# Kernel tuning notes

Measured on AMD Instinct MI355X. Metric: run time of the kernel, lower is better.

The kernel has to match this reference:

```python
import jax, jax.numpy as jnp
import numpy as np

T, H, F, E, K = 4096, 1024, 4096, 8, 2


def setup_inputs() -> dict:
    key = jax.random.key(0)
    ks = jax.random.split(key, 6)
    hidden_states = jax.random.normal(ks[0], (T, H), dtype=jnp.float32)
    expert_weights = jax.random.uniform(ks[1], (T, K), dtype=jnp.float32)
    selected_experts = jax.random.randint(ks[2], (T, K), 0, E, dtype=jnp.int64)
    W1 = 0.02 * jax.random.normal(ks[3], (E, H, F), dtype=jnp.float32)
    b1 = jnp.zeros((E, F), dtype=jnp.float32)
    W2 = 0.02 * jax.random.normal(ks[4], (E, F, H), dtype=jnp.float32)
    b2 = jnp.zeros((E, H), dtype=jnp.float32)
    return {"hidden_states": hidden_states, "expert_weights": expert_weights,
            "W1": W1, "b1": b1, "W2": W2, "b2": b2,
            "selected_experts": selected_experts}


def reference(hidden_states, expert_weights, W1, b1, W2, b2, selected_experts):
    # Combine weight per (token, expert): sum of routing weights over top-k
    # slots assigned to that expert; slots with expert_idx < 0 contribute 0.
    num_experts = W1.shape[0]
    onehot = (selected_experts[:, :, None] == jnp.arange(num_experts)[None, None, :])
    valid = (selected_experts >= 0)[:, :, None]
    cw = jnp.einsum('tk,tke->te', expert_weights,
                    (onehot & valid).astype(hidden_states.dtype))  # [T, E]

    out = jnp.zeros_like(hidden_states)
    for e in range(num_experts):  # small fixed expert count
        h = jax.nn.gelu(hidden_states @ W1[e] + b1[e], approximate=False)  # [T, F]
        y = h @ W2[e] + b2[e]                                              # [T, H]
        out = out + cw[:, e:e + 1] * y
    return out
```

## Files before the change

kernel.cpp:

```cpp
#include <hip/hip_runtime.h>
#include <hip/hip_bf16.h>

#define Td 4096
#define Hd 1024
#define Fd 4096
#define Ed 8
#define Rcap 10240

typedef __attribute__((ext_vector_type(8))) short bf16x8;
typedef __attribute__((ext_vector_type(4))) float f32x4;
typedef __attribute__((ext_vector_type(8))) unsigned short u16x8;

__device__ __forceinline__ unsigned short f32_to_bf16(float x) {
  unsigned int u = __float_as_uint(x);
  unsigned int r = (u + 0x7FFFu + ((u >> 16) & 1u)) >> 16;
  return (unsigned short)r;
}

__device__ __forceinline__ void gload_lds16(const unsigned short* g, unsigned short* l) {
  __builtin_amdgcn_global_load_lds(
      (const __attribute__((address_space(1))) unsigned int*)g,
      (__attribute__((address_space(3))) unsigned int*)l, 16, 0, 0);
}

__global__ __launch_bounds__(256) void cvt_bf16_kernel(const float* __restrict__ in,
                                                       unsigned short* __restrict__ outp, int n8) {
  int i = blockIdx.x * 256 + threadIdx.x;
  if (i >= n8) return;
  const float4* p = (const float4*)(in + (size_t)i * 8);
  float4 a = p[0], b = p[1];
  u16x8 o;
  o[0] = f32_to_bf16(a.x); o[1] = f32_to_bf16(a.y); o[2] = f32_to_bf16(a.z); o[3] = f32_to_bf16(a.w);
  o[4] = f32_to_bf16(b.x); o[5] = f32_to_bf16(b.y); o[6] = f32_to_bf16(b.z); o[7] = f32_to_bf16(b.w);
  *(u16x8*)(outp + (size_t)i * 8) = o;
}

__global__ __launch_bounds__(256) void transpose_cvt_kernel(const float* __restrict__ in,
                                                            unsigned short* __restrict__ outp,
                                                            int Rdm, int Cdm) {
  __shared__ float tile[64][68];
  int tilesR = Rdm >> 6, tilesC = Cdm >> 6;
  int per = tilesR * tilesC;
  int bid = blockIdx.x;
  int e = bid / per; int rem = bid - e * per;
  int tr = rem / tilesC; int tc = rem - tr * tilesC;
  int r0 = tr << 6, c0 = tc << 6;
  int tid = threadIdx.x;
  int rr = tid >> 2, cq = (tid & 3) << 4;
  const float* src = in + ((size_t)e * Rdm + r0 + rr) * Cdm + c0 + cq;
  float4 v0 = ((const float4*)src)[0];
  float4 v1 = ((const float4*)src)[1];
  float4 v2 = ((const float4*)src)[2];
  float4 v3 = ((const float4*)src)[3];
  *(float4*)&tile[rr][cq + 0]  = v0;
  *(float4*)&tile[rr][cq + 4]  = v1;
  *(float4*)&tile[rr][cq + 8]  = v2;
  *(float4*)&tile[rr][cq + 12] = v3;
  __syncthreads();
  u16x8 o0, o1;
#pragma unroll
  for (int j = 0; j < 8; j++) o0[j] = f32_to_bf16(tile[cq + j][rr]);
#pragma unroll
  for (int j = 0; j < 8; j++) o1[j] = f32_to_bf16(tile[cq + 8 + j][rr]);
  unsigned short* dst = outp + ((size_t)e * Cdm + c0 + rr) * Rdm + r0 + cq;
  *(u16x8*)dst = o0;
  *(u16x8*)(dst + 8) = o1;
}

__global__ __launch_bounds__(1024) void route_all_kernel(const int* __restrict__ sel,
                                                         const float* __restrict__ ew,
                                                         int* __restrict__ idxT,
                                                         float* __restrict__ wgtT,
                                                         int* __restrict__ off_g,
                                                         int* __restrict__ cidx,
                                                         float* __restrict__ cwgt) {
  __shared__ int cnt[Ed];
  __shared__ int off[Ed + 1];
  int tid = threadIdx.x;
  if (tid < Ed) cnt[tid] = 0;
  __syncthreads();
  for (int t = tid; t < Td; t += 1024) {
    int e0 = sel[2 * t], e1 = sel[2 * t + 1];
    float w0 = ew[2 * t], w1 = ew[2 * t + 1];
    if (e0 == e1) { w0 += w1; e1 = -1; }
    if (e0 >= 0 && e0 < Ed) { int p = atomicAdd(&cnt[e0], 1); idxT[e0 * Td + p] = t; wgtT[e0 * Td + p] = w0; }
    if (e1 >= 0 && e1 < Ed) { int p = atomicAdd(&cnt[e1], 1); idxT[e1 * Td + p] = t; wgtT[e1 * Td + p] = w1; }
  }
  __syncthreads();
  if (tid == 0) {
    int acc = 0; off[0] = 0;
#pragma unroll
    for (int e = 0; e < Ed; e++) { acc += (cnt[e] + 255) & ~255; off[e + 1] = acc; }
  }
  __syncthreads();
  for (int j = tid; j < Ed * Td; j += 1024) {
    int e = j >> 12, i = j & (Td - 1);
    int row = off[e] + i;
    if (row < off[e + 1]) {
      if (i < cnt[e]) { cidx[row] = idxT[e * Td + i]; cwgt[row] = wgtT[e * Td + i]; }
      else            { cidx[row] = -1;               cwgt[row] = 0.f; }
    }
  }
  if (tid <= Ed) off_g[tid] = off[tid];
}

template <bool FIRST, int KD, int NC, int KSPLIT>
__global__ __launch_bounds__(512, 2) void gemm_kernel(const unsigned short* __restrict__ Abase,
                                                      const unsigned short* __restrict__ Bt,
                                                      const float* __restrict__ bias,
                                                      const int* __restrict__ cidx,
                                                      const float* __restrict__ cwgt,
                                                      const int* __restrict__ off,
                                                      unsigned short* __restrict__ hbuf,
                                                      float* __restrict__ outp) {
  extern __shared__ unsigned short lds[];
  constexpr int KLEN = KD / KSPLIT;
  constexpr int NT = KLEN / 64;

  const int row0 = blockIdx.x << 8;
  const int tot = off[Ed];
  if (row0 >= tot) return;
  int e = 0;
  while (off[e + 1] <= row0) ++e;
  const int n0 = blockIdx.y << 7;
  const int kbase = blockIdx.z * KLEN;

  const int tid = threadIdx.x;
  const int lane = tid & 63, w = tid >> 6;
  const int wrow = w >> 2, wcol = w & 3;
  const int fr = lane & 15;
  const int fkb = (lane >> 4) << 4;

  const unsigned short* aptr[4];
#pragma unroll
  for (int i = 0; i < 4; i++) {
    int r = (i << 6) + (tid >> 3);
    int kel = ((tid & 7) ^ (r & 7)) << 3;
    int g;
    if (FIRST) { g = cidx[row0 + r]; if (g < 0) g = 0; }
    else       { g = row0 + r; }
    aptr[i] = Abase + (size_t)g * KD + kbase + kel;
  }
  const unsigned short* bptr[2];
#pragma unroll
  for (int i = 0; i < 2; i++) {
    int r = (i << 6) + (tid >> 3);
    int kel = ((tid & 7) ^ (r & 7)) << 3;
    bptr[i] = Bt + ((size_t)e * NC + n0 + r) * KD + kbase + kel;
  }
  unsigned short* ldsA = lds;
  unsigned short* ldsB = lds + 49152;

  f32x4 acc[8][2] = {};

#define STAGE(t)                                                         \
  {                                                                      \
    int _b = (t) % 3;                                                    \
    int _k0 = (t) << 6;                                                  \
    unsigned short* _la = ldsA + (_b << 14) + (w << 9);                  \
    unsigned short* _lb = ldsB + (_b << 13) + (w << 9);                  \
    _Pragma("unroll")                                                    \
    for (int _i = 0; _i < 4; _i++) gload_lds16(aptr[_i] + _k0, _la + (_i << 12)); \
    _Pragma("unroll")                                                    \
    for (int _i = 0; _i < 2; _i++) gload_lds16(bptr[_i] + _k0, _lb + (_i << 12)); \
  }

#define LDA(dst, buf, m, ks)                                                     \
  {                                                                              \
    int _r = (wrow << 7) + ((m) << 4) + fr;                                      \
    int _p = (((ks) << 6) + fkb) ^ ((_r & 7) << 4);                              \
    dst = *(const bf16x8*)(ldsA + ((buf) << 14) + (_r << 6) + (_p >> 1));        \
  }
#define LDB(dst, buf, nf, ks)                                                    \
  {                                                                              \
    int _r = (wcol << 5) + ((nf) << 4) + fr;                                     \
    int _p = (((ks) << 6) + fkb) ^ ((_r & 7) << 4);                              \
    dst = *(const bf16x8*)(ldsB + ((buf) << 13) + (_r << 6) + (_p >> 1));        \
  }

  STAGE(0);
  if constexpr (NT > 1) {
    STAGE(1);
    asm volatile("s_waitcnt vmcnt(6)" ::: "memory");
  } else {
    asm volatile("s_waitcnt vmcnt(0)" ::: "memory");
  }
  __builtin_amdgcn_s_barrier();

  for (int t = 0; t < NT; ++t) {
    const int buf = t % 3;
    bf16x8 bfr[2][2];
#pragma unroll
    for (int nf = 0; nf < 2; nf++)
#pragma unroll
      for (int ks = 0; ks < 2; ks++) LDB(bfr[nf][ks], buf, nf, ks);
    bf16x8 afr[4][2];
#pragma unroll
    for (int m = 0; m < 4; m++)
#pragma unroll
      for (int ks = 0; ks < 2; ks++) LDA(afr[m][ks], buf, m, ks);
    if (t + 2 < NT) STAGE(t + 2);
    __builtin_amdgcn_s_barrier();
    __builtin_amdgcn_s_setprio(1);
#pragma unroll
    for (int m = 0; m < 4; m++)
#pragma unroll
      for (int nf = 0; nf < 2; nf++)
#pragma unroll
        for (int ks = 0; ks < 2; ks++)
          acc[m][nf] = __builtin_amdgcn_mfma_f32_16x16x32_bf16(afr[m][ks], bfr[nf][ks], acc[m][nf], 0, 0, 0);
    __builtin_amdgcn_s_setprio(0);
    __builtin_amdgcn_s_barrier();
#pragma unroll
    for (int m = 0; m < 4; m++)
#pragma unroll
      for (int ks = 0; ks < 2; ks++) LDA(afr[m][ks], buf, m + 4, ks);
    __builtin_amdgcn_s_barrier();
    __builtin_amdgcn_s_setprio(1);
#pragma unroll
    for (int m = 0; m < 4; m++)
#pragma unroll
      for (int nf = 0; nf < 2; nf++)
#pragma unroll
        for (int ks = 0; ks < 2; ks++)
          acc[m + 4][nf] = __builtin_amdgcn_mfma_f32_16x16x32_bf16(afr[m][ks], bfr[nf][ks], acc[m + 4][nf], 0, 0, 0);
    __builtin_amdgcn_s_setprio(0);
    if (t + 2 < NT) { asm volatile("s_waitcnt vmcnt(6)" ::: "memory"); }
    else            { asm volatile("s_waitcnt vmcnt(0)" ::: "memory"); }
    __builtin_amdgcn_s_barrier();
  }
#undef STAGE
#undef LDA
#undef LDB

  if (FIRST) {
    float bv[2];
#pragma unroll
    for (int nf = 0; nf < 2; nf++) bv[nf] = bias[e * NC + n0 + (wcol << 5) + (nf << 4) + fr];
#pragma unroll
    for (int m = 0; m < 8; m++) {
#pragma unroll
      for (int r2 = 0; r2 < 4; r2++) {
        int row = row0 + (wrow << 7) + (m << 4) + ((lane >> 4) << 2) + r2;
#pragma unroll
        for (int nf = 0; nf < 2; nf++) {
          int col = n0 + (wcol << 5) + (nf << 4) + fr;
          float x = acc[m][nf][r2] + bv[nf];
          float g = 0.5f * x * (1.0f + erff(x * 0.70710678118654752f));
          hbuf[(size_t)row * NC + col] = f32_to_bf16(g);
        }
      }
    }
  } else {
    float bv[2];
#pragma unroll
    for (int nf = 0; nf < 2; nf++)
      bv[nf] = (blockIdx.z == 0) ? bias[e * NC + n0 + (wcol << 5) + (nf << 4) + fr] : 0.f;
#pragma unroll
    for (int m = 0; m < 8; m++) {
#pragma unroll
      for (int r2 = 0; r2 < 4; r2++) {
        int row = row0 + (wrow << 7) + (m << 4) + ((lane >> 4) << 2) + r2;
        int tdst = cidx[row];
        float cw = cwgt[row];
        if (tdst >= 0) {
#pragma unroll
          for (int nf = 0; nf < 2; nf++) {
            int col = n0 + (wcol << 5) + (nf << 4) + fr;
            atomicAdd(outp + (size_t)tdst * NC + col, cw * (acc[m][nf][r2] + bv[nf]));
          }
        }
      }
    }
  }
}

extern "C" void kernel_launch(void* const* d_in, const int* in_sizes, int n_in,
                              void* d_out, int out_size, void* d_ws, size_t ws_size,
                              hipStream_t stream) {
  const float* hidden = (const float*)d_in[0];
  const float* ew     = (const float*)d_in[1];
  const float* W1     = (const float*)d_in[2];
  const float* b1     = (const float*)d_in[3];
  const float* W2     = (const float*)d_in[4];
  const float* b2     = (const float*)d_in[5];
  const int*   sel    = (const int*)d_in[6];
  float* outp = (float*)d_out;

  unsigned short* hbf  = (unsigned short*)d_ws;
  unsigned short* W1T  = hbf + (size_t)Td * Hd;
  unsigned short* W2T  = W1T + (size_t)Ed * Fd * Hd;
  unsigned short* hbuf = W2T + (size_t)Ed * Hd * Fd;
  int*   idxT = (int*)(hbuf + (size_t)Rcap * Fd);
  float* wgtT = (float*)(idxT + Ed * Td);
  int*   off  = (int*)(wgtT + Ed * Td);
  int*   cidx = off + 16;
  float* cwgt = (float*)(cidx + Rcap);

  constexpr int LDS_BYTES = 147456;
  (void)hipFuncSetAttribute((const void*)gemm_kernel<true, Hd, Fd, 1>,
                            hipFuncAttributeMaxDynamicSharedMemorySize, LDS_BYTES);
  (void)hipFuncSetAttribute((const void*)gemm_kernel<false, Fd, Hd, 2>,
                            hipFuncAttributeMaxDynamicSharedMemorySize, LDS_BYTES);

  (void)hipMemsetAsync(d_out, 0, (size_t)Td * Hd * sizeof(float), stream);

  cvt_bf16_kernel<<<(Td * Hd / 8 + 255) / 256, 256, 0, stream>>>(hidden, hbf, Td * Hd / 8);
  transpose_cvt_kernel<<<Ed * (Hd / 64) * (Fd / 64), 256, 0, stream>>>(W1, W1T, Hd, Fd);
  transpose_cvt_kernel<<<Ed * (Fd / 64) * (Hd / 64), 256, 0, stream>>>(W2, W2T, Fd, Hd);

  route_all_kernel<<<1, 1024, 0, stream>>>(sel, ew, idxT, wgtT, off, cidx, cwgt);

  gemm_kernel<true, Hd, Fd, 1><<<dim3(Rcap / 256, Fd / 128, 1), 512, LDS_BYTES, stream>>>(
      hbf, W1T, b1, cidx, cwgt, off, hbuf, nullptr);
  gemm_kernel<false, Fd, Hd, 2><<<dim3(Rcap / 256, Hd / 128, 2), 512, LDS_BYTES, stream>>>(
      hbuf, W2T, b2, cidx, cwgt, off, nullptr, outp);
}
```

Measured before the change: 658.8 us.

## Replace atomic scatter with per-row output plus combine kernel, retile GEMM warps

```diff
diff --git a/kernel.cpp b/kernel.cpp
--- a/kernel.cpp
+++ b/kernel.cpp
@@ -70,64 +70,77 @@
 __global__ __launch_bounds__(1024) void route_all_kernel(const int* __restrict__ sel,
                                                          const float* __restrict__ ew,
                                                          int* __restrict__ idxT,
-                                                         float* __restrict__ wgtT,
                                                          int* __restrict__ off_g,
                                                          int* __restrict__ cidx,
-                                                         float* __restrict__ cwgt) {
+                                                         int2* __restrict__ trow,
+                                                         float2* __restrict__ twgt) {
   __shared__ int cnt[Ed];
   __shared__ int off[Ed + 1];
   int tid = threadIdx.x;
   if (tid < Ed) cnt[tid] = 0;
   __syncthreads();
-  for (int t = tid; t < Td; t += 1024) {
+  int2 pks[Td / 1024];
+#pragma unroll
+  for (int k = 0; k < Td / 1024; k++) {
+    int t = tid + (k << 10);
     int e0 = sel[2 * t], e1 = sel[2 * t + 1];
     float w0 = ew[2 * t], w1 = ew[2 * t + 1];
     if (e0 == e1) { w0 += w1; e1 = -1; }
-    if (e0 >= 0 && e0 < Ed) { int p = atomicAdd(&cnt[e0], 1); idxT[e0 * Td + p] = t; wgtT[e0 * Td + p] = w0; }
-    if (e1 >= 0 && e1 < Ed) { int p = atomicAdd(&cnt[e1], 1); idxT[e1 * Td + p] = t; wgtT[e1 * Td + p] = w1; }
+    int2 pk = make_int2(-1, -1);
+    if (e0 >= 0 && e0 < Ed) { int p = atomicAdd(&cnt[e0], 1); idxT[e0 * Td + p] = t; pk.x = (p << 3) | e0; }
+    if (e1 >= 0 && e1 < Ed) { int p = atomicAdd(&cnt[e1], 1); idxT[e1 * Td + p] = t; pk.y = (p << 3) | e1; }
+    pks[k] = pk;
+    twgt[t] = make_float2(w0, w1);
   }
   __syncthreads();
   if (tid == 0) {
-    int acc = 0; off[0] = 0;
-#pragma unroll
-    for (int e = 0; e < Ed; e++) { acc += (cnt[e] + 255) & ~255; off[e + 1] = acc; }
+    int a = 0; off[0] = 0;
+#pragma unroll
+    for (int e = 0; e < Ed; e++) { a += (cnt[e] + 255) & ~255; off[e + 1] = a; }
   }
   __syncthreads();
+#pragma unroll
+  for (int k = 0; k < Td / 1024; k++) {
+    int t = tid + (k << 10);
+    int2 pk = pks[k];
+    int2 r;
+    r.x = (pk.x >= 0) ? off[pk.x & 7] + (pk.x >> 3) : -1;
+    r.y = (pk.y >= 0) ? off[pk.y & 7] + (pk.y >> 3) : -1;
+    trow[t] = r;
+  }
   for (int j = tid; j < Ed * Td; j += 1024) {
     int e = j >> 12, i = j & (Td - 1);
     int row = off[e] + i;
-    if (row < off[e + 1]) {
-      if (i < cnt[e]) { cidx[row] = idxT[e * Td + i]; cwgt[row] = wgtT[e * Td + i]; }
-      else            { cidx[row] = -1;               cwgt[row] = 0.f; }
-    }
+    if (row < off[e + 1]) cidx[row] = (i < cnt[e]) ? idxT[e * Td + i] : -1;
   }
   if (tid <= Ed) off_g[tid] = off[tid];
 }
 
-template <bool FIRST, int KD, int NC, int KSPLIT>
-__global__ __launch_bounds__(512, 2) void gemm_kernel(const unsigned short* __restrict__ Abase,
+template <bool FIRST, int KD, int NC, int MAP>
+__global__ __launch_bounds__(512, 1) void gemm_kernel(const unsigned short* __restrict__ Abase,
                                                       const unsigned short* __restrict__ Bt,
                                                       const float* __restrict__ bias,
                                                       const int* __restrict__ cidx,
-                                                      const float* __restrict__ cwgt,
                                                       const int* __restrict__ off,
                                                       unsigned short* __restrict__ hbuf,
-                                                      float* __restrict__ outp) {
+                                                      float* __restrict__ yout) {
   extern __shared__ unsigned short lds[];
-  constexpr int KLEN = KD / KSPLIT;
-  constexpr int NT = KLEN / 64;
-
-  const int row0 = blockIdx.x << 8;
+  constexpr int NT = KD / 64;
+
+  const int xcd = blockIdx.x & 7, slot = blockIdx.x >> 3;
+  int mt, nt;
+  if (MAP == 0) { nt = (xcd << 2) + (slot & 3); mt = slot >> 2; }
+  else          { nt = slot & 7;                mt = xcd * 5 + (slot >> 3); }
+  const int row0 = mt << 8;
   const int tot = off[Ed];
   if (row0 >= tot) return;
   int e = 0;
   while (off[e + 1] <= row0) ++e;
-  const int n0 = blockIdx.y << 7;
-  const int kbase = blockIdx.z * KLEN;
+  const int n0 = nt << 7;
 
   const int tid = threadIdx.x;
   const int lane = tid & 63, w = tid >> 6;
-  const int wrow = w >> 2, wcol = w & 3;
+  const int wrow = w >> 1, wcol = w & 1;
   const int fr = lane & 15;
   const int fkb = (lane >> 4) << 4;
 
@@ -139,140 +152,132 @@
     int g;
     if (FIRST) { g = cidx[row0 + r]; if (g < 0) g = 0; }
     else       { g = row0 + r; }
-    aptr[i] = Abase + (size_t)g * KD + kbase + kel;
+    aptr[i] = Abase + (size_t)g * KD + kel;
   }
   const unsigned short* bptr[2];
 #pragma unroll
   for (int i = 0; i < 2; i++) {
     int r = (i << 6) + (tid >> 3);
     int kel = ((tid & 7) ^ (r & 7)) << 3;
-    bptr[i] = Bt + ((size_t)e * NC + n0 + r) * KD + kbase + kel;
+    bptr[i] = Bt + ((size_t)e * NC + n0 + r) * KD + kel;
   }
   unsigned short* ldsA = lds;
   unsigned short* ldsB = lds + 49152;
 
-  f32x4 acc[8][2] = {};
-
-#define STAGE(t)                                                         \
-  {                                                                      \
-    int _b = (t) % 3;                                                    \
-    int _k0 = (t) << 6;                                                  \
-    unsigned short* _la = ldsA + (_b << 14) + (w << 9);                  \
-    unsigned short* _lb = ldsB + (_b << 13) + (w << 9);                  \
-    _Pragma("unroll")                                                    \
-    for (int _i = 0; _i < 4; _i++) gload_lds16(aptr[_i] + _k0, _la + (_i << 12)); \
-    _Pragma("unroll")                                                    \
-    for (int _i = 0; _i < 2; _i++) gload_lds16(bptr[_i] + _k0, _lb + (_i << 12)); \
-  }
-
-#define LDA(dst, buf, m, ks)                                                     \
-  {                                                                              \
-    int _r = (wrow << 7) + ((m) << 4) + fr;                                      \
-    int _p = (((ks) << 6) + fkb) ^ ((_r & 7) << 4);                              \
-    dst = *(const bf16x8*)(ldsA + ((buf) << 14) + (_r << 6) + (_p >> 1));        \
-  }
-#define LDB(dst, buf, nf, ks)                                                    \
-  {                                                                              \
-    int _r = (wcol << 5) + ((nf) << 4) + fr;                                     \
-    int _p = (((ks) << 6) + fkb) ^ ((_r & 7) << 4);                              \
-    dst = *(const bf16x8*)(ldsB + ((buf) << 13) + (_r << 6) + (_p >> 1));        \
-  }
-
-  STAGE(0);
-  if constexpr (NT > 1) {
-    STAGE(1);
-    asm volatile("s_waitcnt vmcnt(6)" ::: "memory");
-  } else {
-    asm volatile("s_waitcnt vmcnt(0)" ::: "memory");
-  }
+  f32x4 acc[4][4] = {};
+
+#define STAGE_P(t, ph)                                                              \
+  {                                                                                 \
+    const int _b = (t) % 3; const int _k0 = (t) << 6;                               \
+    unsigned short* _la = ldsA + (_b << 14) + ((ph) << 13) + (w << 9);              \
+    unsigned short* _lb = ldsB + (_b << 13) + ((ph) << 12) + (w << 9);              \
+    gload_lds16(aptr[(ph) * 2 + 0] + _k0, _la);                                     \
+    gload_lds16(aptr[(ph) * 2 + 1] + _k0, _la + 4096);                              \
+    gload_lds16(bptr[(ph)] + _k0, _lb);                                             \
+  }
+
+#define LDA(dst, buf, m, ks)                                                        \
+  {                                                                                 \
+    int _r = (wrow << 6) + ((m) << 4) + fr;                                         \
+    int _p = (((ks) << 6) + fkb) ^ ((_r & 7) << 4);                                 \
+    dst = *(const bf16x8*)(ldsA + ((buf) << 14) + (_r << 6) + (_p >> 1));           \
+  }
+#define LDB(dst, buf, nf, ks)                                                       \
+  {                                                                                 \
+    int _r = (wcol << 6) + ((nf) << 4) + fr;                                        \
+    int _p = (((ks) << 6) + fkb) ^ ((_r & 7) << 4);                                 \
+    dst = *(const bf16x8*)(ldsB + ((buf) << 13) + (_r << 6) + (_p >> 1));           \
+  }
+
+  STAGE_P(0, 0); STAGE_P(0, 1);
+  STAGE_P(1, 0); STAGE_P(1, 1);
+  asm volatile("s_waitcnt vmcnt(6)" ::: "memory");
   __builtin_amdgcn_s_barrier();
 
   for (int t = 0; t < NT; ++t) {
     const int buf = t % 3;
-    bf16x8 bfr[2][2];
-#pragma unroll
-    for (int nf = 0; nf < 2; nf++)
-#pragma unroll
-      for (int ks = 0; ks < 2; ks++) LDB(bfr[nf][ks], buf, nf, ks);
-    bf16x8 afr[4][2];
-#pragma unroll
-    for (int m = 0; m < 4; m++)
-#pragma unroll
-      for (int ks = 0; ks < 2; ks++) LDA(afr[m][ks], buf, m, ks);
-    if (t + 2 < NT) STAGE(t + 2);
-    __builtin_amdgcn_s_barrier();
-    __builtin_amdgcn_s_setprio(1);
-#pragma unroll
-    for (int m = 0; m < 4; m++)
-#pragma unroll
-      for (int nf = 0; nf < 2; nf++)
-#pragma unroll
-        for (int ks = 0; ks < 2; ks++)
-          acc[m][nf] = __builtin_amdgcn_mfma_f32_16x16x32_bf16(afr[m][ks], bfr[nf][ks], acc[m][nf], 0, 0, 0);
-    __builtin_amdgcn_s_setprio(0);
-    __builtin_amdgcn_s_barrier();
-#pragma unroll
-    for (int m = 0; m < 4; m++)
-#pragma unroll
-      for (int ks = 0; ks < 2; ks++) LDA(afr[m][ks], buf, m + 4, ks);
-    __builtin_amdgcn_s_barrier();
-    __builtin_amdgcn_s_setprio(1);
-#pragma unroll
-    for (int m = 0; m < 4; m++)
-#pragma unroll
-      for (int nf = 0; nf < 2; nf++)
-#pragma unroll
-        for (int ks = 0; ks < 2; ks++)
-          acc[m + 4][nf] = __builtin_amdgcn_mfma_f32_16x16x32_bf16(afr[m][ks], bfr[nf][ks], acc[m + 4][nf], 0, 0, 0);
-    __builtin_amdgcn_s_setprio(0);
-    if (t + 2 < NT) { asm volatile("s_waitcnt vmcnt(6)" ::: "memory"); }
-    else            { asm volatile("s_waitcnt vmcnt(0)" ::: "memory"); }
-    __builtin_amdgcn_s_barrier();
-  }
-#undef STAGE
+    {
+      bf16x8 af[4], bfr[4];
+#pragma unroll
+      for (int m = 0; m < 4; m++) LDA(af[m], buf, m, 0);
+#pragma unroll
+      for (int n = 0; n < 4; n++) LDB(bfr[n], buf, n, 0);
+      if (t + 2 < NT) STAGE_P(t + 2, 0);
+      __builtin_amdgcn_s_barrier();
+      __builtin_amdgcn_s_setprio(1);
+#pragma unroll
+      for (int m = 0; m < 4; m++)
+#pragma unroll
+        for (int n = 0; n < 4; n++)
+          acc[m][n] = __builtin_amdgcn_mfma_f32_16x16x32_bf16(af[m], bfr[n], acc[m][n], 0, 0, 0);
+      __builtin_amdgcn_s_setprio(0);
+      __builtin_amdgcn_s_barrier();
+    }
+    {
+      bf16x8 af[4], bfr[4];
+#pragma unroll
+      for (int m = 0; m < 4; m++) LDA(af[m], buf, m, 1);
+#pragma unroll
+      for (int n = 0; n < 4; n++) LDB(bfr[n], buf, n, 1);
+      if (t + 2 < NT) STAGE_P(t + 2, 1);
+      __builtin_amdgcn_s_barrier();
+      __builtin_amdgcn_s_setprio(1);
+#pragma unroll
+      for (int m = 0; m < 4; m++)
+#pragma unroll
+        for (int n = 0; n < 4; n++)
+          acc[m][n] = __builtin_amdgcn_mfma_f32_16x16x32_bf16(af[m], bfr[n], acc[m][n], 0, 0, 0);
+      __builtin_amdgcn_s_setprio(0);
+      if (t + 2 < NT) { asm volatile("s_waitcnt vmcnt(6)" ::: "memory"); }
+      else            { asm volatile("s_waitcnt vmcnt(0)" ::: "memory"); }
+      __builtin_amdgcn_s_barrier();
+    }
+  }
+#undef STAGE_P
 #undef LDA
 #undef LDB
 
-  if (FIRST) {
-    float bv[2];
-#pragma unroll
-    for (int nf = 0; nf < 2; nf++) bv[nf] = bias[e * NC + n0 + (wcol << 5) + (nf << 4) + fr];
-#pragma unroll
-    for (int m = 0; m < 8; m++) {
-#pragma unroll
-      for (int r2 = 0; r2 < 4; r2++) {
-        int row = row0 + (wrow << 7) + (m << 4) + ((lane >> 4) << 2) + r2;
-#pragma unroll
-        for (int nf = 0; nf < 2; nf++) {
-          int col = n0 + (wcol << 5) + (nf << 4) + fr;
-          float x = acc[m][nf][r2] + bv[nf];
+  float bv[4];
+#pragma unroll
+  for (int n = 0; n < 4; n++) bv[n] = bias[e * NC + n0 + (wcol << 6) + (n << 4) + fr];
+#pragma unroll
+  for (int m = 0; m < 4; m++) {
+#pragma unroll
+    for (int r2 = 0; r2 < 4; r2++) {
+      int row = row0 + (wrow << 6) + (m << 4) + ((lane >> 4) << 2) + r2;
+#pragma unroll
+      for (int n = 0; n < 4; n++) {
+        int col = n0 + (wcol << 6) + (n << 4) + fr;
+        float x = acc[m][n][r2] + bv[n];
+        if (FIRST) {
           float g = 0.5f * x * (1.0f + erff(x * 0.70710678118654752f));
           hbuf[(size_t)row * NC + col] = f32_to_bf16(g);
+        } else {
+          yout[(size_t)row * NC + col] = x;
         }
       }
     }
-  } else {
-    float bv[2];
-#pragma unroll
-    for (int nf = 0; nf < 2; nf++)
-      bv[nf] = (blockIdx.z == 0) ? bias[e * NC + n0 + (wcol << 5) + (nf << 4) + fr] : 0.f;
-#pragma unroll
-    for (int m = 0; m < 8; m++) {
-#pragma unroll
-      for (int r2 = 0; r2 < 4; r2++) {
-        int row = row0 + (wrow << 7) + (m << 4) + ((lane >> 4) << 2) + r2;
-        int tdst = cidx[row];
-        float cw = cwgt[row];
-        if (tdst >= 0) {
-#pragma unroll
-          for (int nf = 0; nf < 2; nf++) {
-            int col = n0 + (wcol << 5) + (nf << 4) + fr;
-            atomicAdd(outp + (size_t)tdst * NC + col, cw * (acc[m][nf][r2] + bv[nf]));
-          }
-        }
-      }
-    }
-  }
+  }
+}
+
+__global__ __launch_bounds__(256) void combine_kernel(const float* __restrict__ y,
+                                                      const int2* __restrict__ trow,
+                                                      const float2* __restrict__ twgt,
+                                                      float* __restrict__ outp) {
+  int t = blockIdx.x, hq = threadIdx.x;
+  int2 r = trow[t];
+  float2 wv = twgt[t];
+  const float4* y4 = (const float4*)y;
+  float4 a = make_float4(0.f, 0.f, 0.f, 0.f);
+  if (r.x >= 0) {
+    float4 v = y4[(size_t)r.x * (Hd / 4) + hq];
+    a.x = wv.x * v.x; a.y = wv.x * v.y; a.z = wv.x * v.z; a.w = wv.x * v.w;
+  }
+  if (r.y >= 0) {
+    float4 v = y4[(size_t)r.y * (Hd / 4) + hq];
+    a.x += wv.y * v.x; a.y += wv.y * v.y; a.z += wv.y * v.z; a.w += wv.y * v.w;
+  }
+  ((float4*)outp)[(size_t)t * (Hd / 4) + hq] = a;
 }
 
 extern "C" void kernel_launch(void* const* d_in, const int* in_sizes, int n_in,
@@ -291,28 +296,29 @@
   unsigned short* W1T  = hbf + (size_t)Td * Hd;
   unsigned short* W2T  = W1T + (size_t)Ed * Fd * Hd;
   unsigned short* hbuf = W2T + (size_t)Ed * Hd * Fd;
-  int*   idxT = (int*)(hbuf + (size_t)Rcap * Fd);
-  float* wgtT = (float*)(idxT + Ed * Td);
-  int*   off  = (int*)(wgtT + Ed * Td);
-  int*   cidx = off + 16;
-  float* cwgt = (float*)(cidx + Rcap);
+  int*    idxT = (int*)(hbuf + (size_t)Rcap * Fd);
+  int*    off  = idxT + Ed * Td;
+  int*    cidx = off + 16;
+  int2*   trow = (int2*)(cidx + Rcap);
+  float2* twgt = (float2*)(trow + Td);
+  float*  y    = (float*)W1T;
 
   constexpr int LDS_BYTES = 147456;
-  (void)hipFuncSetAttribute((const void*)gemm_kernel<true, Hd, Fd, 1>,
+  (void)hipFuncSetAttribute((const void*)gemm_kernel<true, Hd, Fd, 0>,
                             hipFuncAttributeMaxDynamicSharedMemorySize, LDS_BYTES);
-  (void)hipFuncSetAttribute((const void*)gemm_kernel<false, Fd, Hd, 2>,
+  (void)hipFuncSetAttribute((const void*)gemm_kernel<false, Fd, Hd, 1>,
                             hipFuncAttributeMaxDynamicSharedMemorySize, LDS_BYTES);
-
-  (void)hipMemsetAsync(d_out, 0, (size_t)Td * Hd * sizeof(float), stream);
 
   cvt_bf16_kernel<<<(Td * Hd / 8 + 255) / 256, 256, 0, stream>>>(hidden, hbf, Td * Hd / 8);
   transpose_cvt_kernel<<<Ed * (Hd / 64) * (Fd / 64), 256, 0, stream>>>(W1, W1T, Hd, Fd);
   transpose_cvt_kernel<<<Ed * (Fd / 64) * (Hd / 64), 256, 0, stream>>>(W2, W2T, Fd, Hd);
 
-  route_all_kernel<<<1, 1024, 0, stream>>>(sel, ew, idxT, wgtT, off, cidx, cwgt);
-
-  gemm_kernel<true, Hd, Fd, 1><<<dim3(Rcap / 256, Fd / 128, 1), 512, LDS_BYTES, stream>>>(
-      hbf, W1T, b1, cidx, cwgt, off, hbuf, nullptr);
-  gemm_kernel<false, Fd, Hd, 2><<<dim3(Rcap / 256, Hd / 128, 2), 512, LDS_BYTES, stream>>>(
-      hbuf, W2T, b2, cidx, cwgt, off, nullptr, outp);
-}
+  route_all_kernel<<<1, 1024, 0, stream>>>(sel, ew, idxT, off, cidx, trow, twgt);
+
+  gemm_kernel<true, Hd, Fd, 0><<<1280, 512, LDS_BYTES, stream>>>(
+      hbf, W1T, b1, cidx, off, hbuf, nullptr);
+  gemm_kernel<false, Fd, Hd, 1><<<320, 512, LDS_BYTES, stream>>>(
+      hbuf, W2T, b2, cidx, off, nullptr, y);
+
+  combine_kernel<<<Td, 256, 0, stream>>>(y, trow, twgt, outp);
+}
```

Result: faster. 589.0 us (-10.6%).
